# Optimization experiments

Hardware: AMD Instinct MI355X
Metric: run time of the kernel (lower is better)

## Reference

```python
import jax, jax.numpy as jnp
import numpy as np

NUM_ANGLES = 120
MAX_CONF = 100
FIELD = 50  # prot_field_size L


def setup_inputs() -> dict:
    key = jax.random.key(0)
    ks = jax.random.split(key, 4)
    B = 16
    return {
        "receptor": jax.random.normal(ks[0], (B, 1, FIELD, FIELD), jnp.float32),
        "ligand": jax.random.normal(ks[1], (B, 1, FIELD, FIELD), jnp.float32),
        "w_repr": jax.random.normal(ks[2], (2, 1, 3, 3), jnp.float32) * 0.3,
        "b_repr": jnp.zeros((2,), jnp.float32),
        "w_score": jax.random.normal(ks[3], (1, 4), jnp.float32) * 0.1,
        "b_score": jnp.zeros((1,), jnp.float32),
    }


def reference(receptor, ligand, w_repr, b_repr, w_score, b_score):
    B, _, H, W = receptor.shape  # H = W = FIELD

    # ---- scoring_model.repr : conv(1->2, SAME) + ReLU (stand-in for EQ repr net)
    def repr_net(x):
        y = jax.lax.conv_general_dilated(
            x, w_repr, (1, 1), "SAME", dimension_numbers=("NCHW", "OIHW", "NCHW"))
        return jax.nn.relu(y + b_repr[None, :, None, None])

    rec_feat = repr_net(receptor)  # (B,2,H,W)
    lig_feat = repr_net(ligand)    # (B,2,H,W)

    # ---- rotate: torch affine_grid + grid_sample (bilinear, align_corners=True, zero pad)
    ang = (2.0 * np.pi / NUM_ANGLES) * jnp.arange(NUM_ANGLES, dtype=jnp.float32)
    ca, sa = jnp.cos(ang), jnp.sin(ang)
    lin = jnp.linspace(-1.0, 1.0, H)
    gy, gx = jnp.meshgrid(lin, lin, indexing="ij")  # rows=y, cols=x
    # theta = [[c,-s,0],[s,c,0]] maps output coords -> input coords
    x_in = ca[:, None, None] * gx - sa[:, None, None] * gy  # (A,H,W)
    y_in = sa[:, None, None] * gx + ca[:, None, None] * gy
    px = (x_in + 1.0) * 0.5 * (W - 1)
    py = (y_in + 1.0) * 0.5 * (H - 1)
    x0 = jnp.floor(px).astype(jnp.int32); y0 = jnp.floor(py).astype(jnp.int32)
    x1 = x0 + 1; y1 = y0 + 1
    wx1 = px - x0; wx0 = 1.0 - wx1
    wy1 = py - y0; wy0 = 1.0 - wy1

    def tap(yi, xi, wgt):
        val = lig_feat[:, :, jnp.clip(yi, 0, H - 1), jnp.clip(xi, 0, W - 1)]  # (B,C,A,H,W)
        ok = ((yi >= 0) & (yi < H) & (xi >= 0) & (xi < W)).astype(lig_feat.dtype)
        return val * (wgt * ok)

    lig_rot = (tap(y0, x0, wy0 * wx0) + tap(y0, x1, wy0 * wx1)
               + tap(y1, x0, wy1 * wx0) + tap(y1, x1, wy1 * wx1))
    lig_rot = jnp.transpose(lig_rot, (2, 0, 1, 3, 4))  # (A,B,C,H,W)

    # ---- ProteinConv2D: FFT cross-correlation over all channel pairs, output 2L x 2L
    S = 2 * H
    pad = ((0, 0), (0, 0), (0, H), (0, W))
    Frec = jnp.fft.rfft2(jnp.pad(rec_feat, pad))              # (B,C,S,S/2+1)
    Flig = jnp.fft.rfft2(jnp.pad(lig_rot, ((0, 0),) + pad))   # (A,B,C,S,S/2+1)
    cross = jnp.einsum("bcxy,abdxy->abcdxy", jnp.conj(Frec), Flig)
    A_, C = NUM_ANGLES, rec_feat.shape[1]
    corr = jnp.fft.irfft2(cross.reshape(A_, B, C * C, S, S // 2 + 1), s=(S, S))
    corr = jnp.fft.fftshift(corr, axes=(-2, -1))              # (A,B,4,S,S) centered

    # ---- scoring_model.scorer : Linear(4->1) applied per translation
    scores = jnp.einsum("abcij,c->abij", corr, w_score[0]) + b_score[0]  # (A,B,S,S)

    # ---- update_top: greedy iterative argmin extraction with zero masking
    flat = scores.reshape(A_, B, S * S)

    def greedy(v):
        def step(s, _):
            i = jnp.argmin(s)
            return s.at[i].set(0.0), (i, s[i])
        _, (idx, val) = jax.lax.scan(step, v, None, length=MAX_CONF)
        return idx, val

    idxs, vals = jax.vmap(jax.vmap(greedy))(flat)  # each (A,B,K)

    # ---- final top-1 per batch over all angles/extractions (stable first-min tiebreak)
    K = MAX_CONF
    vals_b = jnp.transpose(vals, (1, 0, 2)).reshape(B, A_ * K)
    j = jnp.argmin(vals_b, axis=1)
    a = j // K
    k = j % K
    pos = idxs[a, jnp.arange(B), k]
    Lf = jnp.float32(S / 2)
    x = (pos // S).astype(jnp.float32)
    y = (pos % S).astype(jnp.float32)
    angles_out = ang[a][:, None]                               # (B,1)
    translations = jnp.stack([x - Lf, y - Lf], axis=1)         # (B,2)
    return angles_out, translations
```

## Files before the change

### kernel.cpp

```cpp
#include <hip/hip_runtime.h>
#include <math.h>

#define NANG 120
#define NB   16
#define H    50
#define SD   100
#define NBIN 51
#define PADB 7
#define BROWS 69
#define BST  106
#define WST  104
#define RTST 52
#define CLAG 100
#define AX   58

__device__ __align__(16) float g_Arec[NB*2*AX*NBIN*2 + 64];
__device__ __align__(16) float g_ligc[NB*2*H*H];
__device__ __align__(16) float g_W[H*WST];
__device__ __align__(16) float g_P[NBIN*128 + 64];
__device__ __align__(16) float g_C[(size_t)NANG*NB*5100];
__device__ unsigned long long g_key[NB];

__device__ const int g_s8[8][2] = {
  {-1,127},{-9,47},{7,-49},{-17,39},{15,-41},{-25,31},{23,127},{-33,127}
};

__global__ __launch_bounds__(512) void k_prep(const float* __restrict__ rec,
                                              const float* __restrict__ lig,
                                              const float* __restrict__ wr,
                                              const float* __restrict__ br,
                                              const float* __restrict__ wsc) {
  const int blk = blockIdx.x;
  const int tid = threadIdx.x;
  if (blk == NB*4) {
    for (int u = tid; u < H*WST; u += 512) {
      int y = u / WST, col = u % WST;
      float v = 0.f;
      if (col < 2*NBIN) {
        int om = col >> 1;
        int k = (om * y) % SD;
        double ang = 6.283185307179586 * (double)k / 100.0;
        v = (col & 1) ? (float)(-sin(ang)) : (float)cos(ang);
      }
      g_W[u] = v;
    }
    for (int u = tid; u < NBIN*128; u += 512) {
      int om = u >> 7, q = u & 127;
      int dy = q >> 1;
      float v = 0.f;
      if (dy <= 49) {
        int k = (om * dy) % SD;
        double ang = 6.283185307179586 * (double)k / 100.0;
        v = (q & 1) ? (float)sin(ang) : (float)cos(ang);
      }
      g_P[u] = v;
    }
    for (int i = tid; i < NB; i += 512) g_key[i] = (0x80000000ULL << 21);
    return;
  }
  const int b = blk >> 2;
  const int part = blk & 3;
  const int omBase = part * 13;
  const int nOm = (part == 3) ? 12 : 13;
  __shared__ float recf[2*H*H];
  __shared__ float tbl[SD*2];
  for (int k = tid; k < SD; k += 512) {
    double ang = 6.283185307179586 * (double)k / 100.0;
    tbl[2*k]   = (float)cos(ang);
    tbl[2*k+1] = (float)sin(ang);
  }
  const float* rimg = rec + b*H*H;
  const float* limg = lig + b*H*H;
  for (int p = tid; p < H*H; p += 512) {
    int i = p / H, j = p - (p/H)*H;
    float ar0 = br[0], ar1 = br[1], al0 = br[0], al1 = br[1];
    for (int di = 0; di < 3; ++di) {
      int ii = i + di - 1;
      if (ii < 0 || ii >= H) continue;
      for (int dj = 0; dj < 3; ++dj) {
        int jj = j + dj - 1;
        if (jj < 0 || jj >= H) continue;
        float rv = rimg[ii*H+jj], lv = limg[ii*H+jj];
        float w0 = wr[di*3 + dj], w1 = wr[9 + di*3 + dj];
        ar0 += w0*rv; ar1 += w1*rv; al0 += w0*lv; al1 += w1*lv;
      }
    }
    ar0 = fmaxf(ar0, 0.f); ar1 = fmaxf(ar1, 0.f);
    recf[p] = ar0; recf[H*H + p] = ar1;
    if (part == 0) {
      al0 = fmaxf(al0, 0.f); al1 = fmaxf(al1, 0.f);
      g_ligc[((b*2+0)*H + i)*H + j] = wsc[0]*al0 + wsc[1]*al1;
      g_ligc[((b*2+1)*H + i)*H + j] = wsc[2]*al0 + wsc[3]*al1;
    }
  }
  if (part == 0) {
    for (int u = tid; u < 2*8*102; u += 512) {
      int c = u / 816; int r = u % 816;
      int x = 50 + r / 102; int q = r % 102;
      g_Arec[((b*2+c)*AX + x)*102 + q] = 0.f;
    }
  }
  __syncthreads();
  for (int u = tid; u < 2*H*nOm; u += 512) {
    int om = omBase + u % nOm;
    int rest = u / nOm; int x = rest % H; int c = rest / H;
    const float* row = recf + (c*H + x)*H;
    float sr = 0.f, si = 0.f;
    int k = 0;
    for (int y = 0; y < H; ++y) {
      float rv = row[y];
      sr += rv * tbl[2*k];
      si -= rv * tbl[2*k+1];
      k += om; if (k >= SD) k -= SD;
    }
    float* dst = g_Arec + ((b*2+c)*AX + x)*102 + 2*om;
    dst[0] = sr; dst[1] = si;
  }
}

#define STEP8(uu) do { \
  float Ar = ar_[(uu)&7], Ai = ai_[(uu)&7]; \
  { const int sl=(uu)&7;     cr0 += Ar*br_[sl]+Ai*bi_[sl]; ci0 += Ar*bi_[sl]-Ai*br_[sl]; } \
  { const int sl=((uu)+1)&7; cr1 += Ar*br_[sl]+Ai*bi_[sl]; ci1 += Ar*bi_[sl]-Ai*br_[sl]; } \
  { const int sl=((uu)+2)&7; cr2 += Ar*br_[sl]+Ai*bi_[sl]; ci2 += Ar*bi_[sl]-Ai*br_[sl]; } \
  { const int sl=((uu)+3)&7; cr3 += Ar*br_[sl]+Ai*bi_[sl]; ci3 += Ar*bi_[sl]-Ai*br_[sl]; } \
  { const int sl=((uu)+4)&7; cr4 += Ar*br_[sl]+Ai*bi_[sl]; ci4 += Ar*bi_[sl]-Ai*br_[sl]; } \
  { const int sl=((uu)+5)&7; cr5 += Ar*br_[sl]+Ai*bi_[sl]; ci5 += Ar*bi_[sl]-Ai*br_[sl]; } \
  { const int sl=((uu)+6)&7; cr6 += Ar*br_[sl]+Ai*bi_[sl]; ci6 += Ar*bi_[sl]-Ai*br_[sl]; } \
  { const int sl=((uu)+7)&7; cr7 += Ar*br_[sl]+Ai*bi_[sl]; ci7 += Ar*bi_[sl]-Ai*br_[sl]; } \
} while(0)

#define TILE8(D0) do { \
  const int d0 = (D0); \
  const int x_lo = max(0, -(d0+7)); \
  const int x_hi = min(H, H - d0); \
  const int ng = (x_hi - x_lo + 7) >> 3; \
  float cr0=0,cr1=0,cr2=0,cr3=0,cr4=0,cr5=0,cr6=0,cr7=0; \
  float ci0=0,ci1=0,ci2=0,ci3=0,ci4=0,ci5=0,ci6=0,ci7=0; \
  _Pragma("unroll 1") \
  for (int c = 0; c < 2; ++c) { \
    const float* Ap = g_Arec + ((b*2+c)*AX + x_lo)*102 + 2*om; \
    const float* Bp = sB + c*(BROWS*BST) + (PADB + x_lo + d0)*BST + 2*om; \
    float br_[8], bi_[8], ar_[8], ai_[8]; \
    _Pragma("unroll") \
    for (int s = 0; s < 8; ++s) { \
      float2 bv = *(const float2*)&Bp[s*BST]; \
      br_[s] = bv.x; bi_[s] = bv.y; \
      float2 av = *(const float2*)&Ap[s*102]; \
      ar_[s] = av.x; ai_[s] = av.y; \
    } \
    _Pragma("unroll 1") \
    for (int g = 0; g < ng-1; ++g) { \
      _Pragma("unroll") \
      for (int u = 0; u < 8; ++u) { \
        STEP8(u); \
        float2 bv = *(const float2*)&Bp[(u+8)*BST]; \
        br_[u] = bv.x; bi_[u] = bv.y; \
        float2 av = *(const float2*)&Ap[(u+8)*102]; \
        ar_[u] = av.x; ai_[u] = av.y; \
      } \
      Bp += 8*BST; Ap += 8*102; \
    } \
    _Pragma("unroll") \
    for (int u = 0; u < 8; ++u) { \
      STEP8(u); \
      if (u < 7) { \
        float2 bv = *(const float2*)&Bp[(u+8)*BST]; \
        br_[u] = bv.x; bi_[u] = bv.y; \
      } \
    } \
  } \
  if (omValid) { \
    const float sc = (om == 0 || om == 50) ? 0.5f : 1.0f; \
    const int base = om*CLAG + (d0 + 49); \
    float* crl = CrL + base; \
    float* gci = g_C + (size_t)bid*5100 + base; \
    float4 v0 = {cr0*sc, cr1*sc, cr2*sc, cr3*sc}; \
    float4 w0 = {ci0*sc, ci1*sc, ci2*sc, ci3*sc}; \
    *(float4*)&crl[0] = v0; \
    *(float4*)&gci[0] = w0; \
    if (d0 != 47) { \
      float4 v1 = {cr4*sc, cr5*sc, cr6*sc, cr7*sc}; \
      float4 w1 = {ci4*sc, ci5*sc, ci6*sc, ci7*sc}; \
      *(float4*)&crl[4] = v1; \
      *(float4*)&gci[4] = w1; \
    } \
  } \
} while(0)

__global__ __launch_bounds__(512, 4) void k_main() {
  const int bid = blockIdx.x;
  const int a = bid % NANG;
  const int b = bid / NANG;
  const int tid = threadIdx.x;

  __shared__ __align__(16) float sMem[19828];
  float* sB  = sMem;
  float* Rt0 = sMem + 14628;
  float* Rt1 = sMem + 17228;
  float* CrL = sMem + 14628;
  float* CiL = sMem;
  float* sP  = sMem + 5100;

  for (int u = tid; u < 2*19*BST; u += 512) {
    int ch = u / (19*BST);
    int r  = (u % (19*BST)) / BST;
    int col = u % BST;
    int row = (r < PADB) ? r : r + 50;
    sB[ch*(BROWS*BST) + row*BST + col] = 0.f;
  }

  float angf = 0.05235987755982988f * (float)a;
  float ca = cosf(angf), sa = sinf(angf);
  const float* L0 = g_ligc + (b*2+0)*H*H;
  const float* L1 = g_ligc + (b*2+1)*H*H;
  for (int p = tid; p < H*H; p += 512) {
    int i = p / H, j = p - (p/H)*H;
    float gy = -1.f + (float)i*(2.f/49.f);
    float gx = -1.f + (float)j*(2.f/49.f);
    float x_in = ca*gx - sa*gy;
    float y_in = sa*gx + ca*gy;
    float px = (x_in + 1.f)*0.5f*49.f;
    float py = (y_in + 1.f)*0.5f*49.f;
    float fx = floorf(px), fy = floorf(py);
    int x0 = (int)fx, y0 = (int)fy;
    int x1 = x0 + 1, y1 = y0 + 1;
    float wx1 = px - fx, wx0 = 1.f - wx1;
    float wy1 = py - fy, wy0 = 1.f - wy1;
    float mx0 = ((unsigned)x0 < (unsigned)H) ? 1.f : 0.f;
    float mx1 = ((unsigned)x1 < (unsigned)H) ? 1.f : 0.f;
    float my0 = ((unsigned)y0 < (unsigned)H) ? 1.f : 0.f;
    float my1 = ((unsigned)y1 < (unsigned)H) ? 1.f : 0.f;
    int x0c = min(max(x0, 0), H-1), x1c = min(max(x1, 0), H-1);
    int y0c = min(max(y0, 0), H-1), y1c = min(max(y1, 0), H-1);
    int o00 = y0c*H + x0c, o01 = y0c*H + x1c;
    int o10 = y1c*H + x0c, o11 = y1c*H + x1c;
    float a00 = L0[o00], a01 = L0[o01], a10 = L0[o10], a11 = L0[o11];
    float b00 = L1[o00], b01 = L1[o01], b10 = L1[o10], b11 = L1[o11];
    float w00 = (wy0*wx0)*(my0*mx0);
    float w01 = (wy0*wx1)*(my0*mx1);
    float w10 = (wy1*wx0)*(my1*mx0);
    float w11 = (wy1*wx1)*(my1*mx1);
    float v0 = 0.f, v1 = 0.f;
    v0 += w00*a00; v1 += w00*b00;
    v0 += w01*a01; v1 += w01*b01;
    v0 += w10*a10; v1 += w10*b10;
    v0 += w11*a11; v1 += w11*b11;
    Rt0[j*RTST + i] = v0;
    Rt1[j*RTST + i] = v1;
  }
  __syncthreads();

  if (tid < 442) {
    int c = tid / 221;
    int r = tid % 221;
    int cg = r % 17;
    int it = r / 17;
    int i0 = it*4;
    int col0 = 6*cg;
    float pacc[4][6];
    #pragma unroll
    for (int p = 0; p < 4; ++p)
      #pragma unroll
      for (int q = 0; q < 6; ++q) pacc[p][q] = 0.f;
    const float* rtc = Rt0 + c*(H*RTST) + i0;
    const float* wt = g_W + col0;
    float wc[5][6];
    #pragma unroll
    for (int yy = 0; yy < 5; ++yy)
      #pragma unroll
      for (int q = 0; q < 3; ++q) {
        float2 w2 = *(const float2*)&wt[yy*WST + 2*q];
        wc[yy][2*q] = w2.x; wc[yy][2*q+1] = w2.y;
      }
    #pragma unroll 1
    for (int yc = 0; yc < 50; yc += 5) {
      float wn[5][6];
      const int yb = (yc + 5 < 50) ? (yc + 5) : 0;
      #pragma unroll
      for (int yy = 0; yy < 5; ++yy)
        #pragma unroll
        for (int q = 0; q < 3; ++q) {
          float2 w2 = *(const float2*)&wt[(yb+yy)*WST + 2*q];
          wn[yy][2*q] = w2.x; wn[yy][2*q+1] = w2.y;
        }
      #pragma unroll
      for (int yy = 0; yy < 5; ++yy) {
        float4 rv = *(const float4*)&rtc[(yc+yy)*RTST];
        float rr[4] = {rv.x, rv.y, rv.z, rv.w};
        #pragma unroll
        for (int p = 0; p < 4; ++p)
          #pragma unroll
          for (int q = 0; q < 6; ++q) pacc[p][q] += rr[p]*wc[yy][q];
      }
      #pragma unroll
      for (int yy = 0; yy < 5; ++yy)
        #pragma unroll
        for (int q = 0; q < 6; ++q) wc[yy][q] = wn[yy][q];
    }
    float* dst = sB + c*(BROWS*BST) + col0;
    #pragma unroll
    for (int p = 0; p < 4; ++p) {
      int i = i0 + p;
      if (i < H) {
        #pragma unroll
        for (int q = 0; q < 3; ++q) {
          float2 o = {pacc[p][2*q], pacc[p][2*q+1]};
          *(float2*)&dst[(PADB+i)*BST + 2*q] = o;
        }
      }
    }
  }
  __syncthreads();

  const int wid = tid >> 6, lane = tid & 63;
  const int om = (lane <= 50) ? lane : 50;
  const bool omValid = (lane <= 50);
  const int d0A = g_s8[wid][0];
  const int d0B = g_s8[wid][1];

  if (d0A != 127) { TILE8(d0A); }
  if (d0B != 127) { TILE8(d0B); }
  __syncthreads();

  {
    const float4* src = (const float4*)(g_C + (size_t)bid*5100);
    float4* dst = (float4*)CiL;
    for (int u = tid; u < 1275; u += 512) dst[u] = src[u];
    for (int u = tid; u < 51*50; u += 512) {
      int o = u / 50, q2 = (u % 50)*2;
      *(float2*)&sP[o*100 + q2] = *(const float2*)&g_P[o*128 + q2];
    }
  }
  __syncthreads();

  float bestV = 3.0e38f; int bestP = 0;
  if (tid < 425) {
    int lt = tid % 25;
    int dt = tid / 25;
    int l0 = 4*lt, dy0 = 3*dt;
    float su[4][3], sv[4][3];
    #pragma unroll
    for (int k = 0; k < 4; ++k)
      #pragma unroll
      for (int j = 0; j < 3; ++j) { su[k][j] = 0.f; sv[k][j] = 0.f; }
    const float* crp = CrL + l0;
    const float* cip = CiL + l0;
    const float* tp = sP + 2*dy0;
    #pragma unroll 3
    for (int om2 = 0; om2 < NBIN; ++om2) {
      float4 c4 = *(const float4*)&crp[om2*CLAG];
      float4 i4 = *(const float4*)&cip[om2*CLAG];
      float2 t0 = *(const float2*)&tp[om2*100];
      float2 t1 = *(const float2*)&tp[om2*100 + 2];
      float2 t2 = *(const float2*)&tp[om2*100 + 4];
      float cc[4] = {c4.x, c4.y, c4.z, c4.w};
      float ii[4] = {i4.x, i4.y, i4.z, i4.w};
      float co[3] = {t0.x, t1.x, t2.x};
      float si[3] = {t0.y, t1.y, t2.y};
      #pragma unroll
      for (int k = 0; k < 4; ++k)
        #pragma unroll
        for (int j = 0; j < 3; ++j) {
          su[k][j] += cc[k]*co[j];
          sv[k][j] += ii[k]*si[j];
        }
    }
    #pragma unroll
    for (int k = 0; k < 4; ++k) {
      int lagIdx = l0 + k;
      if (lagIdx <= 98) {
        int row = lagIdx + 1;
        #pragma unroll
        for (int j = 0; j < 3; ++j) {
          int dy = dy0 + j;
          if (dy <= 49) {
            float vp = su[k][j] - sv[k][j];
            float vm = su[k][j] + sv[k][j];
            int posp = row*SD + (50 + dy);
            int posm = row*SD + (50 - dy);
            if (vp < bestV || (vp == bestV && posp < bestP)) { bestV = vp; bestP = posp; }
            if (vm < bestV || (vm == bestV && posm < bestP)) { bestV = vm; bestP = posm; }
          }
        }
      }
    }
  }

  #pragma unroll
  for (int off = 32; off > 0; off >>= 1) {
    float v2 = __shfl_xor(bestV, off, 64);
    int   p2 = __shfl_xor(bestP, off, 64);
    if (v2 < bestV || (v2 == bestV && p2 < bestP)) { bestV = v2; bestP = p2; }
  }
  if (lane == 0) {
    unsigned int u = __float_as_uint(bestV);
    u = (u & 0x80000000u) ? ~u : (u | 0x80000000u);
    unsigned long long key = ((unsigned long long)u << 21) |
                             ((unsigned long long)(unsigned)a << 14) |
                             (unsigned long long)(unsigned)bestP;
    atomicMin(&g_key[b], key);
  }
}

__global__ void k_final(float* __restrict__ out) {
  int b = threadIdx.x;
  if (b >= NB) return;
  unsigned long long key = g_key[b];
  int a   = (int)((key >> 14) & 127ULL);
  int pos = (int)(key & 16383ULL);
  out[b] = 0.05235987755982988f * (float)a;
  out[NB + 2*b]     = (float)(pos / SD) - 50.f;
  out[NB + 2*b + 1] = (float)(pos % SD) - 50.f;
}

extern "C" void kernel_launch(void* const* d_in, const int* in_sizes, int n_in,
                              void* d_out, int out_size, void* d_ws, size_t ws_size,
                              hipStream_t stream) {
  const float* rec = (const float*)d_in[0];
  const float* lig = (const float*)d_in[1];
  const float* wr  = (const float*)d_in[2];
  const float* br  = (const float*)d_in[3];
  const float* wsc = (const float*)d_in[4];
  (void)in_sizes; (void)n_in; (void)out_size; (void)d_ws; (void)ws_size;
  hipLaunchKernelGGL(k_prep, dim3(NB*4+1), dim3(512), 0, stream, rec, lig, wr, br, wsc);
  hipLaunchKernelGGL(k_main, dim3(NANG*NB), dim3(512), 0, stream);
  hipLaunchKernelGGL(k_final, dim3(1), dim3(64), 0, stream, (float*)d_out);
}
```

Before: 273.7 us.

## Exploit 180-degree rotation symmetry to compute angle pairs from one rotated ligand

Each block now handles angle a and a+60. The a+60 rotation is a 180-degree flip of the a rotation, so its correlation comes from conjugate/reversed-index tiles (TILE8C) over the same shared-memory rotated ligand. This halves the grid and the bilinear rotation plus ligand FFT setup work per angle. In exchange each block does more tile work and a second inverse/argmin pass, and edge-of-grid sampling semantics must match exactly for the flipped angle. The B-tile stride also shrinks to reduce shared memory.

```diff
diff --git a/kernel.cpp b/kernel.cpp
--- a/kernel.cpp
+++ b/kernel.cpp
@@ -2,27 +2,30 @@
 #include <math.h>
 
 #define NANG 120
+#define NANGH 60
 #define NB   16
 #define H    50
 #define SD   100
 #define NBIN 51
 #define PADB 7
 #define BROWS 69
-#define BST  106
+#define BST  102
 #define WST  104
 #define RTST 52
 #define CLAG 100
+#define TST2 104
 #define AX   58
 
 __device__ __align__(16) float g_Arec[NB*2*AX*NBIN*2 + 64];
 __device__ __align__(16) float g_ligc[NB*2*H*H];
 __device__ __align__(16) float g_W[H*WST];
 __device__ __align__(16) float g_P[NBIN*128 + 64];
-__device__ __align__(16) float g_C[(size_t)NANG*NB*5100];
+__device__ __align__(16) float g_C[(size_t)NANGH*NB*15300];
 __device__ unsigned long long g_key[NB];
 
-__device__ const int g_s8[8][2] = {
-  {-1,127},{-9,47},{7,-49},{-17,39},{15,-41},{-25,31},{23,127},{-33,127}
+__device__ const int g_sched2[8][4] = {
+  {-1,-17,-49,999},{248,232,200,999},{-9,15,296,999},{240,264,47,999},
+  {7,-25,208,999},{256,224,-41,999},{23,-33,216,39},{272,280,31,288}
 };
 
 __global__ __launch_bounds__(512) void k_prep(const float* __restrict__ rec,
@@ -48,7 +51,7 @@
       int om = u >> 7, q = u & 127;
       int dy = q >> 1;
       float v = 0.f;
-      if (dy <= 49) {
+      if (dy <= 50) {
         int k = (om * dy) % SD;
         double ang = 6.283185307179586 * (double)k / 100.0;
         v = (q & 1) ? (float)sin(ang) : (float)cos(ang);
@@ -128,6 +131,18 @@
   { const int sl=((uu)+5)&7; cr5 += Ar*br_[sl]+Ai*bi_[sl]; ci5 += Ar*bi_[sl]-Ai*br_[sl]; } \
   { const int sl=((uu)+6)&7; cr6 += Ar*br_[sl]+Ai*bi_[sl]; ci6 += Ar*bi_[sl]-Ai*br_[sl]; } \
   { const int sl=((uu)+7)&7; cr7 += Ar*br_[sl]+Ai*bi_[sl]; ci7 += Ar*bi_[sl]-Ai*br_[sl]; } \
+} while(0)
+
+#define STEP8C(uu) do { \
+  float Ar = ar_[(uu)&7], Ai = ai_[(uu)&7]; \
+  { const int sl=(8-(uu))&7;  cr0 += Ar*br_[sl]-Ai*bi_[sl]; ci0 += Ar*bi_[sl]+Ai*br_[sl]; } \
+  { const int sl=(9-(uu))&7;  cr1 += Ar*br_[sl]-Ai*bi_[sl]; ci1 += Ar*bi_[sl]+Ai*br_[sl]; } \
+  { const int sl=(10-(uu))&7; cr2 += Ar*br_[sl]-Ai*bi_[sl]; ci2 += Ar*bi_[sl]+Ai*br_[sl]; } \
+  { const int sl=(11-(uu))&7; cr3 += Ar*br_[sl]-Ai*bi_[sl]; ci3 += Ar*bi_[sl]+Ai*br_[sl]; } \
+  { const int sl=(12-(uu))&7; cr4 += Ar*br_[sl]-Ai*bi_[sl]; ci4 += Ar*bi_[sl]+Ai*br_[sl]; } \
+  { const int sl=(13-(uu))&7; cr5 += Ar*br_[sl]-Ai*bi_[sl]; ci5 += Ar*bi_[sl]+Ai*br_[sl]; } \
+  { const int sl=(14-(uu))&7; cr6 += Ar*br_[sl]-Ai*bi_[sl]; ci6 += Ar*bi_[sl]+Ai*br_[sl]; } \
+  { const int sl=(15-(uu))&7; cr7 += Ar*br_[sl]-Ai*bi_[sl]; ci7 += Ar*bi_[sl]+Ai*br_[sl]; } \
 } while(0)
 
 #define TILE8(D0) do { \
@@ -174,7 +189,7 @@
     const float sc = (om == 0 || om == 50) ? 0.5f : 1.0f; \
     const int base = om*CLAG + (d0 + 49); \
     float* crl = CrL + base; \
-    float* gci = g_C + (size_t)bid*5100 + base; \
+    float* gci = g_C + (size_t)bid*15300 + base; \
     float4 v0 = {cr0*sc, cr1*sc, cr2*sc, cr3*sc}; \
     float4 w0 = {ci0*sc, ci1*sc, ci2*sc, ci3*sc}; \
     *(float4*)&crl[0] = v0; \
@@ -188,17 +203,96 @@
   } \
 } while(0)
 
+#define TILE8C(E0) do { \
+  const int e0 = (E0); \
+  const int x_lo = max(0, e0 - 49); \
+  const int x_hi = min(H, e0 + 8); \
+  const int ng = (x_hi - x_lo + 7) >> 3; \
+  float cr0=0,cr1=0,cr2=0,cr3=0,cr4=0,cr5=0,cr6=0,cr7=0; \
+  float ci0=0,ci1=0,ci2=0,ci3=0,ci4=0,ci5=0,ci6=0,ci7=0; \
+  _Pragma("unroll 1") \
+  for (int c = 0; c < 2; ++c) { \
+    const float* Ap = g_Arec + ((b*2+c)*AX + x_lo)*102 + 2*om; \
+    const float* Bq = sB + c*(BROWS*BST) + (PADB + e0 - x_lo)*BST + 2*om; \
+    float br_[8], bi_[8], ar_[8], ai_[8]; \
+    _Pragma("unroll") \
+    for (int s = 0; s < 8; ++s) { \
+      float2 bv = *(const float2*)&Bq[s*BST]; \
+      br_[s] = bv.x; bi_[s] = bv.y; \
+      float2 av = *(const float2*)&Ap[s*102]; \
+      ar_[s] = av.x; ai_[s] = av.y; \
+    } \
+    _Pragma("unroll 1") \
+    for (int g = 0; g < ng-1; ++g) { \
+      _Pragma("unroll") \
+      for (int u = 0; u < 8; ++u) { \
+        STEP8C(u); \
+        float2 bv = *(const float2*)&Bq[-(u+1)*BST]; \
+        br_[7-u] = bv.x; bi_[7-u] = bv.y; \
+        float2 av = *(const float2*)&Ap[(u+8)*102]; \
+        ar_[u] = av.x; ai_[u] = av.y; \
+      } \
+      Bq -= 8*BST; Ap += 8*102; \
+    } \
+    { \
+      const int lowcap = -(PADB + e0 - x_lo - 8*(ng-1)); \
+      _Pragma("unroll") \
+      for (int u = 0; u < 8; ++u) { \
+        STEP8C(u); \
+        if (u < 7) { \
+          int off = -(u+1); if (off < lowcap) off = lowcap; \
+          float2 bv = *(const float2*)&Bq[off*BST]; \
+          br_[7-u] = bv.x; bi_[7-u] = bv.y; \
+        } \
+      } \
+    } \
+  } \
+  if (omValid) { \
+    const float sc = (om == 0 || om == 50) ? 0.5f : 1.0f; \
+    const int base = om*CLAG + e0; \
+    float* gwr = g_C + (size_t)bid*15300 + 5100 + base; \
+    float* gwi = gwr + 5100; \
+    float4 v0 = {cr0*sc, cr1*sc, cr2*sc, cr3*sc}; \
+    float4 w0 = {ci0*sc, ci1*sc, ci2*sc, ci3*sc}; \
+    *(float4*)&gwr[0] = v0; \
+    *(float4*)&gwi[0] = w0; \
+    if (e0 != 96) { \
+      float4 v1 = {cr4*sc, cr5*sc, cr6*sc, cr7*sc}; \
+      float4 w1 = {ci4*sc, ci5*sc, ci6*sc, ci7*sc}; \
+      *(float4*)&gwr[4] = v1; \
+      *(float4*)&gwi[4] = w1; \
+    } \
+  } \
+} while(0)
+
+#define WAVE_REDUCE_ATOMIC(ANG) do { \
+  _Pragma("unroll") \
+  for (int off = 32; off > 0; off >>= 1) { \
+    float v2 = __shfl_xor(bestV, off, 64); \
+    int   p2 = __shfl_xor(bestP, off, 64); \
+    if (v2 < bestV || (v2 == bestV && p2 < bestP)) { bestV = v2; bestP = p2; } \
+  } \
+  if (lane == 0) { \
+    unsigned int u = __float_as_uint(bestV); \
+    u = (u & 0x80000000u) ? ~u : (u | 0x80000000u); \
+    unsigned long long key = ((unsigned long long)u << 21) | \
+                             ((unsigned long long)(unsigned)(ANG) << 14) | \
+                             (unsigned long long)(unsigned)bestP; \
+    atomicMin(&g_key[b], key); \
+  } \
+} while(0)
+
 __global__ __launch_bounds__(512, 4) void k_main() {
   const int bid = blockIdx.x;
-  const int a = bid % NANG;
-  const int b = bid / NANG;
+  const int a1 = bid % NANGH;
+  const int b = bid / NANGH;
   const int tid = threadIdx.x;
 
-  __shared__ __align__(16) float sMem[19828];
+  __shared__ __align__(16) float sMem[19276];
   float* sB  = sMem;
-  float* Rt0 = sMem + 14628;
-  float* Rt1 = sMem + 17228;
-  float* CrL = sMem + 14628;
+  float* Rt0 = sMem + 14076;
+  float* Rt1 = sMem + 16676;
+  float* CrL = sMem + 14076;
   float* CiL = sMem;
   float* sP  = sMem + 5100;
 
@@ -210,7 +304,7 @@
     sB[ch*(BROWS*BST) + row*BST + col] = 0.f;
   }
 
-  float angf = 0.05235987755982988f * (float)a;
+  float angf = 0.05235987755982988f * (float)a1;
   float ca = cosf(angf), sa = sinf(angf);
   const float* L0 = g_ligc + (b*2+0)*H*H;
   const float* L1 = g_ligc + (b*2+1)*H*H;
@@ -316,90 +410,149 @@
   const int wid = tid >> 6, lane = tid & 63;
   const int om = (lane <= 50) ? lane : 50;
   const bool omValid = (lane <= 50);
-  const int d0A = g_s8[wid][0];
-  const int d0B = g_s8[wid][1];
-
-  if (d0A != 127) { TILE8(d0A); }
-  if (d0B != 127) { TILE8(d0B); }
+
+  #pragma unroll 1
+  for (int slot = 0; slot < 4; ++slot) {
+    const int v = g_sched2[wid][slot];
+    if (v == 999) break;
+    if (v < 100) { TILE8(v); }
+    else         { TILE8C(v - 200); }
+  }
   __syncthreads();
 
   {
-    const float4* src = (const float4*)(g_C + (size_t)bid*5100);
+    const float4* src = (const float4*)(g_C + (size_t)bid*15300);
     float4* dst = (float4*)CiL;
     for (int u = tid; u < 1275; u += 512) dst[u] = src[u];
-    for (int u = tid; u < 51*50; u += 512) {
-      int o = u / 50, q2 = (u % 50)*2;
-      *(float2*)&sP[o*100 + q2] = *(const float2*)&g_P[o*128 + q2];
-    }
-  }
-  __syncthreads();
-
-  float bestV = 3.0e38f; int bestP = 0;
-  if (tid < 425) {
-    int lt = tid % 25;
-    int dt = tid / 25;
-    int l0 = 4*lt, dy0 = 3*dt;
-    float su[4][3], sv[4][3];
-    #pragma unroll
-    for (int k = 0; k < 4; ++k)
-      #pragma unroll
-      for (int j = 0; j < 3; ++j) { su[k][j] = 0.f; sv[k][j] = 0.f; }
-    const float* crp = CrL + l0;
-    const float* cip = CiL + l0;
-    const float* tp = sP + 2*dy0;
-    #pragma unroll 3
-    for (int om2 = 0; om2 < NBIN; ++om2) {
-      float4 c4 = *(const float4*)&crp[om2*CLAG];
-      float4 i4 = *(const float4*)&cip[om2*CLAG];
-      float2 t0 = *(const float2*)&tp[om2*100];
-      float2 t1 = *(const float2*)&tp[om2*100 + 2];
-      float2 t2 = *(const float2*)&tp[om2*100 + 4];
-      float cc[4] = {c4.x, c4.y, c4.z, c4.w};
-      float ii[4] = {i4.x, i4.y, i4.z, i4.w};
-      float co[3] = {t0.x, t1.x, t2.x};
-      float si[3] = {t0.y, t1.y, t2.y};
+    for (int u = tid; u < 51*51; u += 512) {
+      int o = u / 51, dy = u % 51;
+      *(float2*)&sP[o*TST2 + 2*dy] = *(const float2*)&g_P[o*128 + 2*dy];
+    }
+  }
+  __syncthreads();
+
+  {
+    float bestV = 3.0e38f; int bestP = 0;
+    if (tid < 425) {
+      int lt = tid % 25;
+      int dt = tid / 25;
+      int l0 = 4*lt, dy0 = 3*dt;
+      float su[4][3], sv[4][3];
       #pragma unroll
       for (int k = 0; k < 4; ++k)
         #pragma unroll
-        for (int j = 0; j < 3; ++j) {
-          su[k][j] += cc[k]*co[j];
-          sv[k][j] += ii[k]*si[j];
-        }
-    }
-    #pragma unroll
-    for (int k = 0; k < 4; ++k) {
-      int lagIdx = l0 + k;
-      if (lagIdx <= 98) {
-        int row = lagIdx + 1;
-        #pragma unroll
-        for (int j = 0; j < 3; ++j) {
-          int dy = dy0 + j;
-          if (dy <= 49) {
-            float vp = su[k][j] - sv[k][j];
-            float vm = su[k][j] + sv[k][j];
-            int posp = row*SD + (50 + dy);
-            int posm = row*SD + (50 - dy);
-            if (vp < bestV || (vp == bestV && posp < bestP)) { bestV = vp; bestP = posp; }
-            if (vm < bestV || (vm == bestV && posm < bestP)) { bestV = vm; bestP = posm; }
+        for (int j = 0; j < 3; ++j) { su[k][j] = 0.f; sv[k][j] = 0.f; }
+      const float* crp = CrL + l0;
+      const float* cip = CiL + l0;
+      const float* tp = sP + 2*dy0;
+      #pragma unroll 3
+      for (int om2 = 0; om2 < NBIN; ++om2) {
+        float4 c4 = *(const float4*)&crp[om2*CLAG];
+        float4 i4 = *(const float4*)&cip[om2*CLAG];
+        float2 t0 = *(const float2*)&tp[om2*TST2];
+        float2 t1 = *(const float2*)&tp[om2*TST2 + 2];
+        float2 t2 = *(const float2*)&tp[om2*TST2 + 4];
+        float cc[4] = {c4.x, c4.y, c4.z, c4.w};
+        float ii[4] = {i4.x, i4.y, i4.z, i4.w};
+        float co[3] = {t0.x, t1.x, t2.x};
+        float si[3] = {t0.y, t1.y, t2.y};
+        #pragma unroll
+        for (int k = 0; k < 4; ++k)
+          #pragma unroll
+          for (int j = 0; j < 3; ++j) {
+            su[k][j] += cc[k]*co[j];
+            sv[k][j] += ii[k]*si[j];
+          }
+      }
+      #pragma unroll
+      for (int k = 0; k < 4; ++k) {
+        int lagIdx = l0 + k;
+        if (lagIdx <= 98) {
+          int row = lagIdx + 1;
+          #pragma unroll
+          for (int j = 0; j < 3; ++j) {
+            int dy = dy0 + j;
+            if (dy <= 49) {
+              float vp = su[k][j] - sv[k][j];
+              float vm = su[k][j] + sv[k][j];
+              int posp = row*SD + (50 + dy);
+              int posm = row*SD + (50 - dy);
+              if (vp < bestV || (vp == bestV && posp < bestP)) { bestV = vp; bestP = posp; }
+              if (vm < bestV || (vm == bestV && posm < bestP)) { bestV = vm; bestP = posm; }
+            }
           }
         }
       }
     }
-  }
-
-  #pragma unroll
-  for (int off = 32; off > 0; off >>= 1) {
-    float v2 = __shfl_xor(bestV, off, 64);
-    int   p2 = __shfl_xor(bestP, off, 64);
-    if (v2 < bestV || (v2 == bestV && p2 < bestP)) { bestV = v2; bestP = p2; }
-  }
-  if (lane == 0) {
-    unsigned int u = __float_as_uint(bestV);
-    u = (u & 0x80000000u) ? ~u : (u | 0x80000000u);
-    unsigned long long key = ((unsigned long long)u << 21) |
-                             ((unsigned long long)(unsigned)a << 14) |
-                             (unsigned long long)(unsigned)bestP;
-    atomicMin(&g_key[b], key);
+    WAVE_REDUCE_ATOMIC(a1);
+  }
+  __syncthreads();
+
+  {
+    const float4* s1 = (const float4*)(g_C + (size_t)bid*15300 + 5100);
+    const float4* s2 = (const float4*)(g_C + (size_t)bid*15300 + 10200);
+    float4* d1 = (float4*)CrL;
+    float4* d2 = (float4*)CiL;
+    for (int u = tid; u < 1275; u += 512) { d1[u] = s1[u]; d2[u] = s2[u]; }
+  }
+  __syncthreads();
+
+  {
+    float bestV = 3.0e38f; int bestP = 0;
+    if (tid < 425) {
+      int lt = tid % 25;
+      int dt = tid / 25;
+      int l0 = 4*lt, dy0 = 3*dt;
+      float su[4][3], sv[4][3];
+      #pragma unroll
+      for (int k = 0; k < 4; ++k)
+        #pragma unroll
+        for (int j = 0; j < 3; ++j) { su[k][j] = 0.f; sv[k][j] = 0.f; }
+      const float* crp = CrL + l0;
+      const float* cip = CiL + l0;
+      const float* tp = sP + 2*dy0;
+      #pragma unroll 3
+      for (int om2 = 0; om2 < NBIN; ++om2) {
+        float4 c4 = *(const float4*)&crp[om2*CLAG];
+        float4 i4 = *(const float4*)&cip[om2*CLAG];
+        float2 t0 = *(const float2*)&tp[om2*TST2];
+        float2 t1 = *(const float2*)&tp[om2*TST2 + 2];
+        float2 t2 = *(const float2*)&tp[om2*TST2 + 4];
+        float cc[4] = {c4.x, c4.y, c4.z, c4.w};
+        float ii[4] = {i4.x, i4.y, i4.z, i4.w};
+        float co[3] = {t0.x, t1.x, t2.x};
+        float si[3] = {t0.y, t1.y, t2.y};
+        #pragma unroll
+        for (int k = 0; k < 4; ++k)
+          #pragma unroll
+          for (int j = 0; j < 3; ++j) {
+            su[k][j] += cc[k]*co[j];
+            sv[k][j] += ii[k]*si[j];
+          }
+      }
+      #pragma unroll
+      for (int k = 0; k < 4; ++k) {
+        int e = l0 + k;
+        if (e <= 98) {
+          int row2 = 99 - e;
+          #pragma unroll
+          for (int j = 0; j < 3; ++j) {
+            int dy = dy0 + j;
+            if (dy <= 50) {
+              float vp = su[k][j] - sv[k][j];
+              int posp = row2*SD + (99 - dy);
+              if (vp < bestV || (vp == bestV && posp < bestP)) { bestV = vp; bestP = posp; }
+              if (dy >= 2) {
+                float vm = su[k][j] + sv[k][j];
+                int posm = row2*SD + (dy - 1);
+                if (vm < bestV || (vm == bestV && posm < bestP)) { bestV = vm; bestP = posm; }
+              }
+            }
+          }
+        }
+      }
+    }
+    WAVE_REDUCE_ATOMIC(a1 + 60);
   }
 }
 
@@ -424,6 +577,6 @@
   const float* wsc = (const float*)d_in[4];
   (void)in_sizes; (void)n_in; (void)out_size; (void)d_ws; (void)ws_size;
   hipLaunchKernelGGL(k_prep, dim3(NB*4+1), dim3(512), 0, stream, rec, lig, wr, br, wsc);
-  hipLaunchKernelGGL(k_main, dim3(NANG*NB), dim3(512), 0, stream);
+  hipLaunchKernelGGL(k_main, dim3(NANGH*NB), dim3(512), 0, stream);
   hipLaunchKernelGGL(k_final, dim3(1), dim3(64), 0, stream, (float*)d_out);
 }
```

Result: no change. 272.7 us (-0.4%).
